# Kernel optimization log

Measured on AMD Instinct MI355X. Metric: run time of the kernel, lower is better.

The kernel has to match this reference:

```python
import jax, jax.numpy as jnp
import numpy as np

D_HEAD = 64

def setup_inputs() -> dict:
    key = jax.random.key(0)
    k1, k2, k3, k4, k5 = jax.random.split(key, 5)
    B, S, D, H, Dh = 2, 2048, 1024, 16, D_HEAD
    std = 0.02
    return {
        "residual": jax.random.normal(k1, (B, S, D), dtype=jnp.float32),
        "W_Q": jax.random.normal(k2, (H, Dh, D), dtype=jnp.float32) * std,
        "W_K": jax.random.normal(k3, (H, Dh, D), dtype=jnp.float32) * std,
        "W_V": jax.random.normal(k4, (H, Dh, D), dtype=jnp.float32) * std,
        "W_O": jax.random.normal(k5, (H, Dh, D), dtype=jnp.float32) * std,
    }

def reference(residual, W_Q, W_K, W_V, W_O):
    # residual: [b, s, d]; W_*: [h, e, d] with e = d_head
    S = residual.shape[1]
    q = jnp.einsum('bsd,hed->bshe', residual, W_Q)
    k = jnp.einsum('bsd,hed->bshe', residual, W_K)
    v = jnp.einsum('bsd,hed->bshe', residual, W_V)
    scale = 1.0 / jnp.sqrt(jnp.asarray(D_HEAD, dtype=residual.dtype))
    scores = jnp.einsum('bqhe,bkhe->bhqk', q, k) * scale  # [b,h,s,s]
    causal = jnp.tril(jnp.ones((S, S), dtype=bool))
    scores = jnp.where(causal, scores, -jnp.inf)
    pattern = jax.nn.softmax(scores, axis=-1)
    attn_out = jnp.einsum('bhqk,bkhe->bqhe', pattern, v)
    out = jnp.einsum('bqhe,hed->bqd', attn_out, W_O)
    return out
```

## Files before the change

### kernel.cpp

```cpp
#include <hip/hip_runtime.h>
#include <math.h>

typedef unsigned short bf16;
typedef unsigned long long u64;
typedef __attribute__((ext_vector_type(8))) short short8;
typedef __attribute__((ext_vector_type(4))) short s16x4;
typedef __attribute__((ext_vector_type(4))) float f32x4;

#define S_LEN 2048
#define NH    16
#define DH    64
#define DM    1024
#define BATCH 2

__device__ __forceinline__ bf16 f2bf(float f) {
    unsigned u = __float_as_uint(f);
    u += 0x7fffu + ((u >> 16) & 1u);
    return (bf16)(u >> 16);
}

__device__ __forceinline__ unsigned pack2(float a, float b) {
    unsigned ua = __float_as_uint(a) + 0x8000u;
    unsigned ub = __float_as_uint(b) + 0x8000u;
    return (ua >> 16) | (ub & 0xFFFF0000u);
}

__device__ __forceinline__ u64 pack4(f32x4 v) {
    return (u64)pack2(v[0], v[1]) | ((u64)pack2(v[2], v[3]) << 32);
}

__device__ __forceinline__ s16x4 pack4s(f32x4 v) {
    union { uint2 u; s16x4 s; } cv;
    cv.u = make_uint2(pack2(v[0], v[1]), pack2(v[2], v[3]));
    return cv.s;
}

__device__ __forceinline__ float fast_exp2(float x) {
#if __has_builtin(__builtin_amdgcn_exp2f)
    return __builtin_amdgcn_exp2f(x);
#else
    return exp2f(x);
#endif
}

__device__ __forceinline__ void gload_lds16(const void* g, void* s) {
    __builtin_amdgcn_global_load_lds(
        (const __attribute__((address_space(1))) unsigned int*)g,
        (__attribute__((address_space(3))) unsigned int*)s, 16, 0, 0);
}

#define QSCALE 0.18033688011112042f

__global__ __launch_bounds__(256) void convert_kernel(
    const float* __restrict__ X,  const float* __restrict__ WQ,
    const float* __restrict__ WK, const float* __restrict__ WV,
    const float* __restrict__ WO,
    bf16* __restrict__ Xb, bf16* __restrict__ WQb, bf16* __restrict__ WKb,
    bf16* __restrict__ WVb, bf16* __restrict__ WOt)
{
    __shared__ float T[64][65];
    const int blk = blockIdx.x;
    if (blk < 7168) {
        const int t = blk * 256 + threadIdx.x;
        if (t < 1048576) {
            float4 v = ((const float4*)X)[t];
            u64 pk = (u64)f2bf(v.x) | ((u64)f2bf(v.y) << 16)
                   | ((u64)f2bf(v.z) << 32) | ((u64)f2bf(v.w) << 48);
            *(u64*)(Xb + 4 * (size_t)t) = pk;
        } else if (t < 1310720) {
            int i = t - 1048576;
            float4 v = ((const float4*)WQ)[i];
            u64 pk = (u64)f2bf(v.x * QSCALE) | ((u64)f2bf(v.y * QSCALE) << 16)
                   | ((u64)f2bf(v.z * QSCALE) << 32) | ((u64)f2bf(v.w * QSCALE) << 48);
            *(u64*)(WQb + 4 * (size_t)i) = pk;
        } else if (t < 1572864) {
            int i = t - 1310720;
            float4 v = ((const float4*)WK)[i];
            u64 pk = (u64)f2bf(v.x) | ((u64)f2bf(v.y) << 16)
                   | ((u64)f2bf(v.z) << 32) | ((u64)f2bf(v.w) << 48);
            *(u64*)(WKb + 4 * (size_t)i) = pk;
        } else {
            int i = t - 1572864;
            float4 v = ((const float4*)WV)[i];
            u64 pk = (u64)f2bf(v.x) | ((u64)f2bf(v.y) << 16)
                   | ((u64)f2bf(v.z) << 32) | ((u64)f2bf(v.w) << 48);
            *(u64*)(WVb + 4 * (size_t)i) = pk;
        }
    } else {
        const int tile = blk - 7168;
        const int he0 = (tile & 15) * 64, d0 = (tile >> 4) * 64;
        const int tid = threadIdx.x;
        const int row = tid >> 2, c0 = (tid & 3) * 16;
        #pragma unroll
        for (int u = 0; u < 4; ++u) {
            float4 v = *(const float4*)(WO + (size_t)(he0 + row) * DM + d0 + c0 + u * 4);
            T[row][c0 + u * 4 + 0] = v.x;
            T[row][c0 + u * 4 + 1] = v.y;
            T[row][c0 + u * 4 + 2] = v.z;
            T[row][c0 + u * 4 + 3] = v.w;
        }
        __syncthreads();
        bf16 tmp[16];
        #pragma unroll
        for (int j = 0; j < 16; ++j) tmp[j] = f2bf(T[c0 + j][row]);
        *(short8*)(WOt + (size_t)(d0 + row) * DM + he0 + c0)     = *(short8*)&tmp[0];
        *(short8*)(WOt + (size_t)(d0 + row) * DM + he0 + c0 + 8) = *(short8*)&tmp[8];
    }
}

__global__ __launch_bounds__(256) void proj_kernel(
    const bf16* __restrict__ Xb, const bf16* __restrict__ WQb,
    const bf16* __restrict__ WKb, const bf16* __restrict__ WVb,
    bf16* __restrict__ qbuf, bf16* __restrict__ kbuf, bf16* __restrict__ vt)
{
    __shared__ char lds[65536];

    const int id = blockIdx.x;
    const int tid = threadIdx.x, wave = tid >> 6, lane = tid & 63;
    const int tx = lane & 15, quad = lane >> 4;
    const int wm = (wave >> 1) * 64, wn = (wave & 1) * 64;

    int mode, am0, bn0, bb = 0;
    const bf16 *Aop, *Bop;
    if (id < 512) {
        mode = id & 1;
        int rem = id >> 1;
        bn0 = (rem & 31) * 128;
        am0 = (rem >> 5) * 128;
        Aop = (mode ? WKb : WQb) + (size_t)am0 * DM;
        Bop = Xb + (size_t)bn0 * DM;
    } else {
        mode = 2;
        int rem = id - 512;
        bb = rem & 1;
        rem >>= 1;
        bn0 = (rem & 7) * 128;
        am0 = (rem >> 3) * 128;
        Aop = Xb + ((size_t)bb * S_LEN + am0) * DM;
        Bop = WVb + (size_t)bn0 * DM;
    }

    f32x4 acc[4][4] = {};

    {
        char* As = lds;
        char* Bs = lds + 16384;
        #pragma unroll
        for (int r = 0; r < 4; ++r) {
            int slot = r * 256 + tid;
            int row = slot >> 3, g = slot & 7, gl = g ^ (row & 7);
            gload_lds16(Aop + (size_t)row * DM + gl * 8, As + r * 4096 + wave * 1024);
            gload_lds16(Bop + (size_t)row * DM + gl * 8, Bs + r * 4096 + wave * 1024);
        }
    }

    for (int kt = 0; kt < 16; ++kt) {
        char* As = lds + (kt & 1) * 32768;
        char* Bs = As + 16384;
        __syncthreads();

        if (kt < 15) {
            char* An = lds + ((kt + 1) & 1) * 32768;
            char* Bn = An + 16384;
            const int k0 = (kt + 1) * 64;
            #pragma unroll
            for (int r = 0; r < 4; ++r) {
                int slot = r * 256 + tid;
                int row = slot >> 3, g = slot & 7, gl = g ^ (row & 7);
                gload_lds16(Aop + (size_t)row * DM + k0 + gl * 8,
                            An + r * 4096 + wave * 1024);
                gload_lds16(Bop + (size_t)row * DM + k0 + gl * 8,
                            Bn + r * 4096 + wave * 1024);
            }
        }

        #pragma unroll
        for (int ks = 0; ks < 2; ++ks) {
            const int swz = ((ks * 4 + quad) ^ (tx & 7)) * 16;
            short8 af[4], bfr[4];
            #pragma unroll
            for (int mt = 0; mt < 4; ++mt)
                af[mt] = *(const short8*)(As + (wm + mt * 16 + tx) * 128 + swz);
            #pragma unroll
            for (int nt = 0; nt < 4; ++nt)
                bfr[nt] = *(const short8*)(Bs + (wn + nt * 16 + tx) * 128 + swz);
            #pragma unroll
            for (int mt = 0; mt < 4; ++mt)
                #pragma unroll
                for (int nt = 0; nt < 4; ++nt)
                    acc[mt][nt] = __builtin_amdgcn_mfma_f32_16x16x32_bf16(
                        af[mt], bfr[nt], acc[mt][nt], 0, 0, 0);
        }
    }

    if (mode < 2) {
        bf16* outb = mode ? kbuf : qbuf;
        #pragma unroll
        for (int mt = 0; mt < 4; ++mt)
            #pragma unroll
            for (int nt = 0; nt < 4; ++nt) {
                int heG  = am0 + wm + mt * 16 + quad * 4;
                int tokG = bn0 + wn + nt * 16 + tx;
                int b = tokG >> 11, s = tokG & 2047;
                int h = heG >> 6, e0 = heG & 63;
                *(u64*)(outb + ((size_t)(b * NH + h) * S_LEN + s) * DH + e0) =
                    pack4(acc[mt][nt]);
            }
    } else {
        #pragma unroll
        for (int mt = 0; mt < 4; ++mt)
            #pragma unroll
            for (int nt = 0; nt < 4; ++nt) {
                int sG  = am0 + wm + mt * 16 + quad * 4;
                int heG = bn0 + wn + nt * 16 + tx;
                *(u64*)(vt + ((size_t)bb * DM + heG) * S_LEN + sG) =
                    pack4(acc[mt][nt]);
            }
    }
}

__global__ __launch_bounds__(256) void flash_kernel(
    const bf16* __restrict__ qbuf, const bf16* __restrict__ kbuf,
    const bf16* __restrict__ vtb, bf16* __restrict__ attn)
{
    __shared__ char lds[32768];

    const int i  = blockIdx.x;
    const int bh = i & 31;
    const int j  = i >> 5;
    const int qb = (i < 256) ? (15 - j) : (j - 8);
    const int tid = threadIdx.x, wave = tid >> 6, lane = tid & 63;
    const int tx = lane & 15, quad = lane >> 4;
    const int sw = tx & 7;

    const bf16* Qg = qbuf + (size_t)bh * S_LEN * DH + (size_t)qb * 128 * DH;
    const bf16* Kg = kbuf + (size_t)bh * S_LEN * DH;
    const bf16* Vg = vtb  + (size_t)bh * DH * S_LEN;

    short8 bq[2][2];
    #pragma unroll
    for (int g = 0; g < 2; ++g)
        #pragma unroll
        for (int es = 0; es < 2; ++es)
            bq[g][es] = *(const short8*)(Qg + (size_t)(wave * 32 + g * 16 + tx) * DH +
                                         (es * 4 + quad) * 8);

    f32x4 oacc[2][4] = {};
    float l_part[2] = {0.0f, 0.0f};

    const int kmax  = 2 * qb + 1;
    const int wdiag = 2 * qb + (wave >> 1);
    const int qg0   = qb * 128 + wave * 32 + tx;

    #pragma unroll
    for (int r = 0; r < 2; ++r) {
        int slot = r * 256 + tid;
        int row = slot >> 3, g = slot & 7, gl = g ^ (row & 7);
        gload_lds16(Kg + (size_t)row * DH + gl * 8, lds + r * 4096 + wave * 1024);
        gload_lds16(Vg + (size_t)row * S_LEN + gl * 8,
                    lds + 8192 + r * 4096 + wave * 1024);
    }

    for (int kt64 = 0; kt64 <= kmax; ++kt64) {
        char* Kc = lds + (kt64 & 1) * 16384;
        char* Vc = Kc + 8192;
        __syncthreads();

        if (kt64 < kmax) {
            char* Kn = lds + ((kt64 + 1) & 1) * 16384;
            char* Vn = Kn + 8192;
            #pragma unroll
            for (int r = 0; r < 2; ++r) {
                int slot = r * 256 + tid;
                int row = slot >> 3, g = slot & 7, gl = g ^ (row & 7);
                gload_lds16(Kg + ((size_t)(kt64 + 1) * 64 + row) * DH + gl * 8,
                            Kn + r * 4096 + wave * 1024);
                gload_lds16(Vg + (size_t)row * S_LEN + (kt64 + 1) * 64 + gl * 8,
                            Vn + r * 4096 + wave * 1024);
            }
        }

        if (kt64 <= wdiag) {
            f32x4 st[2][4] = {};
            #pragma unroll
            for (int es = 0; es < 2; ++es) {
                #pragma unroll
                for (int kt = 0; kt < 4; ++kt) {
                    short8 ak = *(const short8*)(Kc + (kt * 16 + tx) * 128 +
                                                 (((es * 4 + quad) ^ sw) * 16));
                    #pragma unroll
                    for (int g = 0; g < 2; ++g)
                        st[g][kt] = __builtin_amdgcn_mfma_f32_16x16x32_bf16(
                            ak, bq[g][es], st[g][kt], 0, 0, 0);
                }
            }

            if (kt64 == wdiag) {
                #pragma unroll
                for (int g = 0; g < 2; ++g)
                    #pragma unroll
                    for (int kt = 0; kt < 4; ++kt)
                        #pragma unroll
                        for (int r = 0; r < 4; ++r)
                            if (kt64 * 64 + kt * 16 + quad * 4 + r > qg0 + g * 16)
                                st[g][kt][r] = -1e30f;
            }

            s16x4 pb[2][4];
            #pragma unroll
            for (int g = 0; g < 2; ++g) {
                float rs = 0.0f;
                #pragma unroll
                for (int kt = 0; kt < 4; ++kt) {
                    #pragma unroll
                    for (int r = 0; r < 4; ++r) {
                        float p = fast_exp2(st[g][kt][r]);
                        st[g][kt][r] = p;
                        rs += p;
                    }
                    pb[g][kt] = pack4s(st[g][kt]);
                }
                l_part[g] += rs;
            }

            #pragma unroll
            for (int kt = 0; kt < 4; ++kt) {
                #pragma unroll
                for (int et = 0; et < 4; ++et) {
                    s16x4 av = *(const s16x4*)(Vc + (et * 16 + tx) * 128 +
                                 (((kt * 2 + (quad >> 1)) ^ sw) * 16) + (quad & 1) * 8);
                    #pragma unroll
                    for (int g = 0; g < 2; ++g)
                        oacc[g][et] = __builtin_amdgcn_mfma_f32_16x16x16bf16_1k(
                            av, pb[g][kt], oacc[g][et], 0, 0, 0);
                }
            }
        }
    }

    const int b = bh >> 4, h = bh & 15;
    char* Pw = lds + wave * 4096;
    #pragma unroll
    for (int g = 0; g < 2; ++g) {
        float l = l_part[g];
        l += __shfl_xor(l, 16);
        l += __shfl_xor(l, 32);
        float inv = 1.0f / l;
        #pragma unroll
        for (int et = 0; et < 4; ++et) {
            unsigned lo = pack2(oacc[g][et][0] * inv, oacc[g][et][1] * inv);
            unsigned hi = pack2(oacc[g][et][2] * inv, oacc[g][et][3] * inv);
            int eg = et * 2 + (quad >> 1);
            *(uint2*)(Pw + (g * 16 + tx) * 128 + ((eg ^ sw) * 16) +
                      (quad & 1) * 8) = make_uint2(lo, hi);
        }
    }
    asm volatile("s_waitcnt lgkmcnt(0)" ::: "memory");

    #pragma unroll
    for (int g = 0; g < 2; ++g) {
        const int s = qb * 128 + wave * 32 + g * 16 + tx;
        bf16* op = attn + ((size_t)b * S_LEN + s) * DM + h * DH;
        #pragma unroll
        for (int c2 = 0; c2 < 2; ++c2) {
            int c = quad + c2 * 4;
            short8 v = *(const short8*)(Pw + (g * 16 + tx) * 128 + ((c ^ sw) * 16));
            *(short8*)(op + c * 8) = v;
        }
    }
}

__global__ __launch_bounds__(256) void out_proj_kernel(
    const bf16* __restrict__ A, const bf16* __restrict__ Bt,
    float* __restrict__ out)
{
    __shared__ char lds[49152];

    const int m0 = blockIdx.x * 128, n0 = blockIdx.y * 64;
    const int tid = threadIdx.x, wave = tid >> 6, lane = tid & 63;
    const int tx = lane & 15, quad = lane >> 4;
    const int wm = wave * 32;

    f32x4 acc[2][4] = {};

    {
        char* As = lds;
        char* Bs = lds + 16384;
        #pragma unroll
        for (int r = 0; r < 4; ++r) {
            int slot = r * 256 + tid;
            int row = slot >> 3, g = slot & 7, gl = g ^ (row & 7);
            gload_lds16(A + (size_t)(m0 + row) * DM + gl * 8,
                        As + r * 4096 + wave * 1024);
        }
        #pragma unroll
        for (int r = 0; r < 2; ++r) {
            int slot = r * 256 + tid;
            int row = slot >> 3, g = slot & 7, gl = g ^ (row & 7);
            gload_lds16(Bt + (size_t)(n0 + row) * DM + gl * 8,
                        Bs + r * 4096 + wave * 1024);
        }
    }

    for (int kt = 0; kt < 16; ++kt) {
        char* As = lds + (kt & 1) * 24576;
        char* Bs = As + 16384;
        __syncthreads();

        if (kt < 15) {
            char* An = lds + ((kt + 1) & 1) * 24576;
            char* Bn = An + 16384;
            const int k0 = (kt + 1) * 64;
            #pragma unroll
            for (int r = 0; r < 4; ++r) {
                int slot = r * 256 + tid;
                int row = slot >> 3, g = slot & 7, gl = g ^ (row & 7);
                gload_lds16(A + (size_t)(m0 + row) * DM + k0 + gl * 8,
                            An + r * 4096 + wave * 1024);
            }
            #pragma unroll
            for (int r = 0; r < 2; ++r) {
                int slot = r * 256 + tid;
                int row = slot >> 3, g = slot & 7, gl = g ^ (row & 7);
                gload_lds16(Bt + (size_t)(n0 + row) * DM + k0 + gl * 8,
                            Bn + r * 4096 + wave * 1024);
            }
        }

        #pragma unroll
        for (int ks = 0; ks < 2; ++ks) {
            const int swz = ((ks * 4 + quad) ^ (tx & 7)) * 16;
            short8 af[2], bfr[4];
            #pragma unroll
            for (int mt = 0; mt < 2; ++mt)
                af[mt] = *(const short8*)(As + (wm + mt * 16 + tx) * 128 + swz);
            #pragma unroll
            for (int nt = 0; nt < 4; ++nt)
                bfr[nt] = *(const short8*)(Bs + (nt * 16 + tx) * 128 + swz);
            #pragma unroll
            for (int mt = 0; mt < 2; ++mt)
                #pragma unroll
                for (int nt = 0; nt < 4; ++nt)
                    acc[mt][nt] = __builtin_amdgcn_mfma_f32_16x16x32_bf16(
                        af[mt], bfr[nt], acc[mt][nt], 0, 0, 0);
        }
    }

    #pragma unroll
    for (int mt = 0; mt < 2; ++mt)
        #pragma unroll
        for (int nt = 0; nt < 4; ++nt)
            #pragma unroll
            for (int r = 0; r < 4; ++r) {
                int mG = m0 + wm + mt * 16 + quad * 4 + r;
                int nG = n0 + nt * 16 + tx;
                out[(size_t)mG * DM + nG] = acc[mt][nt][r];
            }
}

extern "C" void kernel_launch(void* const* d_in, const int* in_sizes, int n_in,
                              void* d_out, int out_size, void* d_ws, size_t ws_size,
                              hipStream_t stream) {
    const float* X  = (const float*)d_in[0];
    const float* WQ = (const float*)d_in[1];
    const float* WK = (const float*)d_in[2];
    const float* WV = (const float*)d_in[3];
    const float* WO = (const float*)d_in[4];
    float* out = (float*)d_out;

    char* ws = (char*)d_ws;
    bf16* Xb   = (bf16*)(ws);
    bf16* WQb  = (bf16*)(ws + (8u  << 20));
    bf16* WKb  = (bf16*)(ws + (10u << 20));
    bf16* WVb  = (bf16*)(ws + (12u << 20));
    bf16* WOt  = (bf16*)(ws + (14u << 20));
    bf16* qbuf = (bf16*)(ws + (16u << 20));
    bf16* kbuf = (bf16*)(ws + (24u << 20));
    bf16* vt   = (bf16*)(ws + (32u << 20));
    bf16* attn = (bf16*)(ws + (40u << 20));

    convert_kernel<<<7424, 256, 0, stream>>>(X, WQ, WK, WV, WO,
                                             Xb, WQb, WKb, WVb, WOt);
    proj_kernel<<<768, 256, 0, stream>>>(Xb, WQb, WKb, WVb, qbuf, kbuf, vt);
    flash_kernel<<<512, 256, 0, stream>>>(qbuf, kbuf, vt, attn);
    out_proj_kernel<<<dim3(32, 16), 256, 0, stream>>>(attn, WOt, out);
}
```

Before: 169.8 us.

## Shrink flash attention query tile to 64 rows and double grid size

The flash kernel now handles 64 query rows per block (16 per wave) instead of 128, launching 1024 blocks instead of 512, and drops the per-wave diagonal skip logic. This raises block count for better CU occupancy and load balance across the causal triangle. In exchange each block reloads K/V tiles for half as many queries, doubling K/V traffic through LDS, and the output staging buffer now reuses the idle double-buffer half.

```diff
diff --git a/kernel.cpp b/kernel.cpp
--- a/kernel.cpp
+++ b/kernel.cpp
@@ -228,29 +228,26 @@
     const int i  = blockIdx.x;
     const int bh = i & 31;
     const int j  = i >> 5;
-    const int qb = (i < 256) ? (15 - j) : (j - 8);
+    const int qb = (i < 512) ? (31 - j) : (j - 16);
     const int tid = threadIdx.x, wave = tid >> 6, lane = tid & 63;
     const int tx = lane & 15, quad = lane >> 4;
     const int sw = tx & 7;
 
-    const bf16* Qg = qbuf + (size_t)bh * S_LEN * DH + (size_t)qb * 128 * DH;
+    const bf16* Qg = qbuf + (size_t)bh * S_LEN * DH + (size_t)qb * 64 * DH;
     const bf16* Kg = kbuf + (size_t)bh * S_LEN * DH;
     const bf16* Vg = vtb  + (size_t)bh * DH * S_LEN;
 
-    short8 bq[2][2];
+    short8 bq[2];
     #pragma unroll
-    for (int g = 0; g < 2; ++g)
-        #pragma unroll
-        for (int es = 0; es < 2; ++es)
-            bq[g][es] = *(const short8*)(Qg + (size_t)(wave * 32 + g * 16 + tx) * DH +
-                                         (es * 4 + quad) * 8);
-
-    f32x4 oacc[2][4] = {};
-    float l_part[2] = {0.0f, 0.0f};
-
-    const int kmax  = 2 * qb + 1;
-    const int wdiag = 2 * qb + (wave >> 1);
-    const int qg0   = qb * 128 + wave * 32 + tx;
+    for (int es = 0; es < 2; ++es)
+        bq[es] = *(const short8*)(Qg + (size_t)(wave * 16 + tx) * DH +
+                                  (es * 4 + quad) * 8);
+
+    f32x4 oacc[4] = {};
+    float l_part = 0.0f;
+
+    const int kmax = qb;
+    const int qg0  = qb * 64 + wave * 16 + tx;
 
     #pragma unroll
     for (int r = 0; r < 2; ++r) {
@@ -280,93 +277,76 @@
             }
         }
 
-        if (kt64 <= wdiag) {
-            f32x4 st[2][4] = {};
-            #pragma unroll
-            for (int es = 0; es < 2; ++es) {
+        f32x4 st[4] = {};
+        #pragma unroll
+        for (int es = 0; es < 2; ++es) {
+            #pragma unroll
+            for (int kt = 0; kt < 4; ++kt) {
+                short8 ak = *(const short8*)(Kc + (kt * 16 + tx) * 128 +
+                                             (((es * 4 + quad) ^ sw) * 16));
+                st[kt] = __builtin_amdgcn_mfma_f32_16x16x32_bf16(
+                    ak, bq[es], st[kt], 0, 0, 0);
+            }
+        }
+
+        if (kt64 == kmax) {
+            #pragma unroll
+            for (int kt = 0; kt < 4; ++kt)
                 #pragma unroll
-                for (int kt = 0; kt < 4; ++kt) {
-                    short8 ak = *(const short8*)(Kc + (kt * 16 + tx) * 128 +
-                                                 (((es * 4 + quad) ^ sw) * 16));
-                    #pragma unroll
-                    for (int g = 0; g < 2; ++g)
-                        st[g][kt] = __builtin_amdgcn_mfma_f32_16x16x32_bf16(
-                            ak, bq[g][es], st[g][kt], 0, 0, 0);
-                }
-            }
-
-            if (kt64 == wdiag) {
-                #pragma unroll
-                for (int g = 0; g < 2; ++g)
-                    #pragma unroll
-                    for (int kt = 0; kt < 4; ++kt)
-                        #pragma unroll
-                        for (int r = 0; r < 4; ++r)
-                            if (kt64 * 64 + kt * 16 + quad * 4 + r > qg0 + g * 16)
-                                st[g][kt][r] = -1e30f;
-            }
-
-            s16x4 pb[2][4];
-            #pragma unroll
-            for (int g = 0; g < 2; ++g) {
-                float rs = 0.0f;
-                #pragma unroll
-                for (int kt = 0; kt < 4; ++kt) {
-                    #pragma unroll
-                    for (int r = 0; r < 4; ++r) {
-                        float p = fast_exp2(st[g][kt][r]);
-                        st[g][kt][r] = p;
-                        rs += p;
-                    }
-                    pb[g][kt] = pack4s(st[g][kt]);
-                }
-                l_part[g] += rs;
-            }
-
-            #pragma unroll
-            for (int kt = 0; kt < 4; ++kt) {
-                #pragma unroll
-                for (int et = 0; et < 4; ++et) {
-                    s16x4 av = *(const s16x4*)(Vc + (et * 16 + tx) * 128 +
-                                 (((kt * 2 + (quad >> 1)) ^ sw) * 16) + (quad & 1) * 8);
-                    #pragma unroll
-                    for (int g = 0; g < 2; ++g)
-                        oacc[g][et] = __builtin_amdgcn_mfma_f32_16x16x16bf16_1k(
-                            av, pb[g][kt], oacc[g][et], 0, 0, 0);
-                }
+                for (int r = 0; r < 4; ++r)
+                    if (kt64 * 64 + kt * 16 + quad * 4 + r > qg0)
+                        st[kt][r] = -1e30f;
+        }
+
+        s16x4 pb[4];
+        float rs = 0.0f;
+        #pragma unroll
+        for (int kt = 0; kt < 4; ++kt) {
+            #pragma unroll
+            for (int r = 0; r < 4; ++r) {
+                float p = fast_exp2(st[kt][r]);
+                st[kt][r] = p;
+                rs += p;
+            }
+            pb[kt] = pack4s(st[kt]);
+        }
+        l_part += rs;
+
+        #pragma unroll
+        for (int kt = 0; kt < 4; ++kt) {
+            #pragma unroll
+            for (int et = 0; et < 4; ++et) {
+                s16x4 av = *(const s16x4*)(Vc + (et * 16 + tx) * 128 +
+                             (((kt * 2 + (quad >> 1)) ^ sw) * 16) + (quad & 1) * 8);
+                oacc[et] = __builtin_amdgcn_mfma_f32_16x16x16bf16_1k(
+                    av, pb[kt], oacc[et], 0, 0, 0);
             }
         }
     }
 
     const int b = bh >> 4, h = bh & 15;
-    char* Pw = lds + wave * 4096;
+    char* Pw = lds + ((kmax & 1) ^ 1) * 16384 + wave * 2048;
+    float l = l_part;
+    l += __shfl_xor(l, 16);
+    l += __shfl_xor(l, 32);
+    float inv = 1.0f / l;
     #pragma unroll
-    for (int g = 0; g < 2; ++g) {
-        float l = l_part[g];
-        l += __shfl_xor(l, 16);
-        l += __shfl_xor(l, 32);
-        float inv = 1.0f / l;
-        #pragma unroll
-        for (int et = 0; et < 4; ++et) {
-            unsigned lo = pack2(oacc[g][et][0] * inv, oacc[g][et][1] * inv);
-            unsigned hi = pack2(oacc[g][et][2] * inv, oacc[g][et][3] * inv);
-            int eg = et * 2 + (quad >> 1);
-            *(uint2*)(Pw + (g * 16 + tx) * 128 + ((eg ^ sw) * 16) +
-                      (quad & 1) * 8) = make_uint2(lo, hi);
-        }
+    for (int et = 0; et < 4; ++et) {
+        unsigned lo = pack2(oacc[et][0] * inv, oacc[et][1] * inv);
+        unsigned hi = pack2(oacc[et][2] * inv, oacc[et][3] * inv);
+        int eg = et * 2 + (quad >> 1);
+        *(uint2*)(Pw + tx * 128 + ((eg ^ sw) * 16) + (quad & 1) * 8) =
+            make_uint2(lo, hi);
     }
     asm volatile("s_waitcnt lgkmcnt(0)" ::: "memory");
 
+    const int s = qb * 64 + wave * 16 + tx;
+    bf16* op = attn + ((size_t)b * S_LEN + s) * DM + h * DH;
     #pragma unroll
-    for (int g = 0; g < 2; ++g) {
-        const int s = qb * 128 + wave * 32 + g * 16 + tx;
-        bf16* op = attn + ((size_t)b * S_LEN + s) * DM + h * DH;
-        #pragma unroll
-        for (int c2 = 0; c2 < 2; ++c2) {
-            int c = quad + c2 * 4;
-            short8 v = *(const short8*)(Pw + (g * 16 + tx) * 128 + ((c ^ sw) * 16));
-            *(short8*)(op + c * 8) = v;
-        }
+    for (int c2 = 0; c2 < 2; ++c2) {
+        int c = quad + c2 * 4;
+        short8 v = *(const short8*)(Pw + tx * 128 + ((c ^ sw) * 16));
+        *(short8*)(op + c * 8) = v;
     }
 }
 
@@ -482,6 +462,6 @@
     convert_kernel<<<7424, 256, 0, stream>>>(X, WQ, WK, WV, WO,
                                              Xb, WQb, WKb, WVb, WOt);
     proj_kernel<<<768, 256, 0, stream>>>(Xb, WQb, WKb, WVb, qbuf, kbuf, vt);
-    flash_kernel<<<512, 256, 0, stream>>>(qbuf, kbuf, vt, attn);
+    flash_kernel<<<1024, 256, 0, stream>>>(qbuf, kbuf, vt, attn);
     out_proj_kernel<<<dim3(32, 16), 256, 0, stream>>>(attn, WOt, out);
 }
```

After: 160.9 us. 1.06x faster.
